# Performance work log

Measured on AMD Instinct MI355X. Metric: run time of the kernel, lower is better.

## Reference

```python
import jax, jax.numpy as jnp
import numpy as np

N = 50000        # nodes
E = 800000       # edges
FEAT = 64        # cfg.feature_dim
HID = 128        # cfg.hidden_dim
G = 8            # num graphs
EPS = 1e-5       # LayerNorm eps
MIN_DEPTH, MAX_DEPTH = 0.1, 3.0


def _ln(x, g, b):
    m = jnp.mean(x, axis=-1, keepdims=True)
    v = jnp.mean((x - m) ** 2, axis=-1, keepdims=True)
    return (x - m) * jax.lax.rsqrt(v + EPS) * g + b


def setup_inputs() -> dict:
    key = jax.random.key(0)
    ks = jax.random.split(key, 32)
    f32 = jnp.float32
    inp = {}
    inp['x'] = jax.random.normal(ks[0], (N, FEAT), dtype=f32)
    inp['edge_index'] = jax.random.randint(ks[1], (2, E), 0, N)
    inp['batch'] = jnp.sort(jax.random.randint(ks[2], (N,), 0, G))
    # input_projection: Linear(FEAT,HID) + LayerNorm
    inp['in_w'] = jax.random.normal(ks[3], (FEAT, HID), dtype=f32) * (1.0 / np.sqrt(FEAT))
    inp['in_b'] = jnp.zeros((HID,), f32)
    inp['in_ln_g'] = jnp.ones((HID,), f32)
    inp['in_ln_b'] = jnp.zeros((HID,), f32)
    # epigenetics
    inp['methylation'] = jnp.zeros((HID,), f32)
    inp['histones'] = jnp.zeros((4,), f32)
    inp['log_depth'] = jnp.zeros((), f32)
    # NeuralODEFunc: 3 stacked GCNConv(HID,HID) + LayerNorms, gate MLP, residual scalar
    inp['gcn_w'] = jax.random.normal(ks[4], (3, HID, HID), dtype=f32) * (1.0 / np.sqrt(HID))
    inp['gcn_b'] = jnp.zeros((3, HID), f32)
    inp['ln_g'] = jnp.ones((3, HID), f32)
    inp['ln_b'] = jnp.zeros((3, HID), f32)
    inp['gate_w'] = jax.random.normal(ks[5], (2 * HID, HID), dtype=f32) * (1.0 / np.sqrt(2 * HID))
    inp['gate_b'] = jnp.zeros((HID,), f32)
    inp['residual_weight'] = jnp.asarray(0.1, f32)
    # output_projection: Linear(HID,HID) + LayerNorm
    inp['out_w'] = jax.random.normal(ks[6], (HID, HID), dtype=f32) * (1.0 / np.sqrt(HID))
    inp['out_b'] = jnp.zeros((HID,), f32)
    inp['out_ln_g'] = jnp.ones((HID,), f32)
    inp['out_ln_b'] = jnp.zeros((HID,), f32)
    return inp


def reference(x, edge_index, batch, in_w, in_b, in_ln_g, in_ln_b, methylation,
              histones, log_depth, gcn_w, gcn_b, ln_g, ln_b, gate_w, gate_b,
              residual_weight, out_w, out_b, out_ln_g, out_ln_b):
    n = x.shape[0]
    src, dst = edge_index[0], edge_index[1]

    # input_projection (Dropout is identity in eval)
    h = jax.nn.relu(_ln(x @ in_w + in_b, in_ln_g, in_ln_b))

    # epigenetic regulation (chromatin_accessibility goes through .item() -> constant)
    meth_sil = jnp.mean(jax.nn.sigmoid(methylation))
    hm = jax.nn.sigmoid(histones)
    act = (hm[0] + hm[2]) * 0.5
    rep = (hm[1] + hm[3]) * 0.5
    chrom = jax.lax.stop_gradient(jnp.clip(act - rep + 0.5, 0.0, 1.0))
    h = h * (chrom * (1.0 - meth_sil))

    # symmetric GCN normalization, no self loops (computed once, no grad path)
    deg = jax.ops.segment_sum(jnp.ones((E,), h.dtype), dst, num_segments=n)
    dinv = jnp.where(deg > 0, jax.lax.rsqrt(jnp.maximum(deg, 1.0)), 0.0)
    enorm = (dinv[src] * dinv[dst])[:, None]  # [E,1]

    def gcn(hh, i):
        xw = hh @ gcn_w[i]                                   # [N,H]
        agg = jax.ops.segment_sum(xw[src] * enorm, dst, num_segments=n)
        return agg + gcn_b[i]

    def ode_f(hh):
        h_orig = hh
        cur = hh
        for i in range(3):  # fixed layer count
            h_new = _ln(gcn(cur, i), ln_g[i], ln_b[i])
            if i > 0:
                gate = jax.nn.sigmoid(
                    jnp.concatenate([cur, h_new], axis=-1) @ gate_w + gate_b)
                cur = gate * h_new + (1.0 - gate) * cur
            else:
                cur = h_new
        cur = jnp.tanh(cur)
        return cur + residual_weight * h_orig

    # depth via .item() in torch -> non-differentiable constant
    depth = jax.lax.stop_gradient(
        jnp.clip(jnp.exp(log_depth), MIN_DEPTH, MAX_DEPTH))
    # single fixed RK4 step over t = linspace(0, depth, 2)
    dt = depth
    k1 = ode_f(h)
    k2 = ode_f(h + 0.5 * dt * k1)
    k3 = ode_f(h + 0.5 * dt * k2)
    k4 = ode_f(h + dt * k3)
    h_final = h + (dt / 6.0) * (k1 + 2.0 * k2 + 2.0 * k3 + k4)

    # output_projection + global_mean_pool over batch
    h_out = _ln(h_final @ out_w + out_b, out_ln_g, out_ln_b)
    cnt = jax.ops.segment_sum(jnp.ones((n,), h.dtype), batch, num_segments=G)
    pooled = jax.ops.segment_sum(h_out, batch, num_segments=G)
    return pooled / jnp.maximum(cnt, 1.0)[:, None]
```

## Files before the change

kernel.cpp:

```cpp
#include <hip/hip_runtime.h>
#include <math.h>

#define NN 50000
#define EE 800000
#define HH 128
#define FF 64
#define GG 8
#define PB 500

using short8 = __attribute__((ext_vector_type(8))) short;
using f32x4  = __attribute__((ext_vector_type(4))) float;

__device__ __forceinline__ float sigm(float x){ return 1.0f/(1.0f+expf(-x)); }
__device__ __forceinline__ unsigned short f2bf(float f){
    union { float f; unsigned u; } v; v.f = f;
    unsigned r = v.u + 0x7fff + ((v.u >> 16) & 1);
    return (unsigned short)(r >> 16);
}
__device__ __forceinline__ float bf2f(unsigned short h){
    union { unsigned u; float f; } v; v.u = ((unsigned)h) << 16;
    return v.f;
}

__global__ void k_setup(const float* __restrict__ meth,
                        const float* __restrict__ histones,
                        const float* __restrict__ logd,
                        float* __restrict__ scal)
{
    int l = threadIdx.x;
    float s = sigm(meth[l]) + sigm(meth[l + 64]);
#pragma unroll
    for (int o = 32; o >= 1; o >>= 1) s += __shfl_xor(s, o, 64);
    if (l == 0) {
        float msil = s * (1.0f / 128.0f);
        float h0 = sigm(histones[0]), h1 = sigm(histones[1]);
        float h2 = sigm(histones[2]), h3 = sigm(histones[3]);
        float act = (h0 + h2) * 0.5f, rep = (h1 + h3) * 0.5f;
        float chrom = fminf(fmaxf(act - rep + 0.5f, 0.0f), 1.0f);
        scal[0] = chrom * (1.0f - msil);
        float d = expf(logd[0]);
        scal[1] = fminf(fmaxf(d, 0.1f), 3.0f);
    }
}

__global__ void k_pack(const float* __restrict__ W, unsigned short* __restrict__ out, int K)
{
    int i = blockIdx.x * 256 + threadIdx.x;
    if (i >= K * 128) return;
    int k = i >> 7, n = i & 127;
    int c = k >> 5, kl = k & 31, q = kl >> 3, j = kl & 7;
    int b = n >> 4, ln = n & 15;
    int lane = q * 16 + ln;
    out[((c * 8 + b) * 64 + lane) * 8 + j] = f2bf(W[i]);
}

__global__ void k_cvtx(const float* __restrict__ x, unsigned short* __restrict__ xb)
{
    size_t i = (size_t)blockIdx.x * 256 + threadIdx.x;
    if (i >= (size_t)NN * 16) return;
    float4 v = ((const float4*)x)[i];
    ushort4 o;
    o.x = f2bf(v.x); o.y = f2bf(v.y); o.z = f2bf(v.z); o.w = f2bf(v.w);
    ((ushort4*)xb)[i] = o;
}

__global__ void k_hist(const int* __restrict__ ei, int* __restrict__ hist)
{
    int e = blockIdx.x * 256 + threadIdx.x;
    if (e < EE) atomicAdd(&hist[ei[EE + e]], 1);
}

__global__ void k_dinv(const int* __restrict__ hist, float* __restrict__ dinv)
{
    int n = blockIdx.x * 256 + threadIdx.x;
    if (n < NN) {
        int d = hist[n];
        dinv[n] = d > 0 ? rsqrtf((float)d) : 0.0f;
    }
}

__global__ void k_scan_a(const int* __restrict__ hist, int* __restrict__ aux)
{
    __shared__ int sh[256];
    int b = blockIdx.x, t = threadIdx.x;
    int base = b * 1024 + t * 4;
    int s = 0;
#pragma unroll
    for (int j = 0; j < 4; ++j) { int i = base + j; if (i < NN) s += hist[i]; }
    sh[t] = s; __syncthreads();
    for (int o = 128; o >= 1; o >>= 1) { if (t < o) sh[t] += sh[t + o]; __syncthreads(); }
    if (t == 0) aux[b] = sh[0];
}

__global__ void k_scan_b(int* __restrict__ aux, int nb)
{
    if (blockIdx.x == 0 && threadIdx.x == 0) {
        int run = 0;
        for (int i = 0; i < nb; ++i) { int v = aux[i]; aux[i] = run; run += v; }
    }
}

__global__ void k_scan_c(const int* __restrict__ hist, const int* __restrict__ aux,
                         int* __restrict__ row_ptr)
{
    __shared__ int sh[256];
    int b = blockIdx.x, t = threadIdx.x;
    int base = b * 1024 + t * 4;
    int v[4]; int s = 0;
#pragma unroll
    for (int j = 0; j < 4; ++j) { int i = base + j; v[j] = (i < NN) ? hist[i] : 0; s += v[j]; }
    sh[t] = s; __syncthreads();
    for (int o = 1; o < 256; o <<= 1) {
        int x = 0; if (t >= o) x = sh[t - o];
        __syncthreads(); sh[t] += x; __syncthreads();
    }
    int run = aux[b] + sh[t] - s;
#pragma unroll
    for (int j = 0; j < 4; ++j) { int i = base + j; if (i < NN) row_ptr[i] = run; run += v[j]; }
    if (b == 0 && t == 0) row_ptr[NN] = EE;
}

__global__ void k_scatter(const int* __restrict__ ei, const float* __restrict__ dinv,
                          int* __restrict__ cursor, int2* __restrict__ ew)
{
    int e = blockIdx.x * 256 + threadIdx.x;
    if (e >= EE) return;
    int s = ei[e], d = ei[EE + e];
    int p = atomicAdd(&cursor[d], 1);
    ew[p] = make_int2(s, __float_as_int(dinv[s] * dinv[d]));
}

__global__ void k_bounds(const int* __restrict__ batch, int* __restrict__ st)
{
    int g = threadIdx.x;
    if (g > GG) return;
    int lo = 0, hi = NN;
    while (lo < hi) { int mid = (lo + hi) >> 1; if (batch[mid] < g) lo = mid + 1; else hi = mid; }
    st[g] = lo;
}

template<int KC, int MODE>
__global__ __launch_bounds__(256) void k_dense_mfma(
    const unsigned short* __restrict__ A, const unsigned short* __restrict__ Wp,
    const float* __restrict__ bias, const float* __restrict__ lng,
    const float* __restrict__ lnb, const float* __restrict__ scal,
    unsigned short* __restrict__ out)
{
    __shared__ unsigned short Ws[KC * 4096];
    const int t = threadIdx.x;
    {
        const float4* src = (const float4*)Wp;
        float4* dst = (float4*)Ws;
#pragma unroll
        for (int i = 0; i < KC * 2; ++i) dst[t + i * 256] = src[t + i * 256];
    }
    __syncthreads();
    const int wave = t >> 6, lane = t & 63;
    const int quad = lane >> 4, ln = lane & 15;
    const int r0 = blockIdx.x * 64 + wave * 16;
    const int K = KC * 32;
    const int arow = r0 + ln;
    const bool av = arow < NN;

    f32x4 acc[8] = {};
#pragma unroll
    for (int c = 0; c < KC; ++c) {
        short8 a = {};
        if (av) a = *(const short8*)(A + (size_t)arow * K + c * 32 + quad * 8);
#pragma unroll
        for (int b = 0; b < 8; ++b) {
            short8 bb = *(const short8*)&Ws[((c * 8 + b) * 64 + lane) * 8];
            acc[b] = __builtin_amdgcn_mfma_f32_16x16x32_bf16(a, bb, acc[b], 0, 0, 0);
        }
    }

    float b_s[8], g_s[8], e_s[8];
#pragma unroll
    for (int b = 0; b < 8; ++b) {
        int col = b * 16 + ln;
        b_s[b] = bias[col]; g_s[b] = lng[col]; e_s[b] = lnb[col];
    }
    float sc = (MODE == 1) ? scal[0] : 0.0f;
#pragma unroll
    for (int i = 0; i < 4; ++i) {
        int row = r0 + quad * 4 + i;
        float v[8]; float s = 0.f, q = 0.f;
#pragma unroll
        for (int b = 0; b < 8; ++b) { float x = acc[b][i] + b_s[b]; v[b] = x; s += x; q += x * x; }
#pragma unroll
        for (int o = 1; o < 16; o <<= 1) { s += __shfl_xor(s, o, 64); q += __shfl_xor(q, o, 64); }
        float m  = s * (1.0f / 128.0f);
        float vr = q * (1.0f / 128.0f) - m * m;
        float rs = rsqrtf(vr + 1e-5f);
        if (row < NN) {
#pragma unroll
            for (int b = 0; b < 8; ++b) {
                float o2 = (v[b] - m) * rs * g_s[b] + e_s[b];
                if (MODE == 1) o2 = fmaxf(o2, 0.f) * sc;
                out[(size_t)row * 128 + b * 16 + ln] = f2bf(o2);
            }
        }
    }
}

__global__ __launch_bounds__(256) void k_gate_mfma(
    unsigned short* __restrict__ cur, const unsigned short* __restrict__ hnew,
    const unsigned short* __restrict__ Wp, const float* __restrict__ gb)
{
    __shared__ unsigned short Ws[16384];
    const int t = threadIdx.x;
    const int wave = t >> 6, lane = t & 63;
    const int quad = lane >> 4, ln = lane & 15;
    const int r0 = blockIdx.x * 64 + wave * 16;
    const int arow = r0 + ln;
    const bool av = arow < NN;

    f32x4 acc[8] = {};
#pragma unroll
    for (int s = 0; s < 2; ++s) {
        __syncthreads();
        {
            const float4* src = (const float4*)(Wp + (size_t)s * 16384);
            float4* dst = (float4*)Ws;
#pragma unroll
            for (int i = 0; i < 8; ++i) dst[t + i * 256] = src[t + i * 256];
        }
        __syncthreads();
        const unsigned short* A = s ? hnew : cur;
#pragma unroll
        for (int c = 0; c < 4; ++c) {
            short8 a = {};
            if (av) a = *(const short8*)(A + (size_t)arow * 128 + c * 32 + quad * 8);
#pragma unroll
            for (int b = 0; b < 8; ++b) {
                short8 bb = *(const short8*)&Ws[((c * 8 + b) * 64 + lane) * 8];
                acc[b] = __builtin_amdgcn_mfma_f32_16x16x32_bf16(a, bb, acc[b], 0, 0, 0);
            }
        }
    }

    float gb_s[8];
#pragma unroll
    for (int b = 0; b < 8; ++b) gb_s[b] = gb[b * 16 + ln];
#pragma unroll
    for (int i = 0; i < 4; ++i) {
        int row = r0 + quad * 4 + i;
        if (row < NN) {
#pragma unroll
            for (int b = 0; b < 8; ++b) {
                size_t idx = (size_t)row * 128 + b * 16 + ln;
                float g  = sigm(acc[b][i] + gb_s[b]);
                float cu = bf2f(cur[idx]);
                float hn = bf2f(hnew[idx]);
                cur[idx] = f2bf(g * hn + (1.f - g) * cu);
            }
        }
    }
}

__global__ __launch_bounds__(256) void k_spmm(
    const int* __restrict__ rp, const int2* __restrict__ ew,
    const unsigned short* __restrict__ X, unsigned short* __restrict__ out)
{
    const int wave = threadIdx.x >> 6, lane = threadIdx.x & 63;
    const int node = blockIdx.x * 4 + wave;
    const int beg = rp[node], end = rp[node + 1];
    float2 acc = make_float2(0.f, 0.f);
    const unsigned short* Xl = X + lane * 2;

    for (int base = beg; base < end; base += 64) {
        const int cnt = min(64, end - base);
        int2 my = make_int2(0, 0);
        if (lane < cnt) my = ew[base + lane];
        const int cq = (cnt + 7) & ~7;
        for (int j = 0; j < cq; j += 8) {
            float2 v[8]; float wv[8];
#pragma unroll
            for (int u = 0; u < 8; ++u) {
                int s  = __shfl(my.x, j + u, 64);
                wv[u]  = __int_as_float(__shfl(my.y, j + u, 64));
                ushort2 r = *(const ushort2*)(Xl + (size_t)s * 128);
                v[u] = make_float2(bf2f(r.x), bf2f(r.y));
            }
#pragma unroll
            for (int u = 0; u < 8; ++u) {
                acc.x = fmaf(wv[u], v[u].x, acc.x);
                acc.y = fmaf(wv[u], v[u].y, acc.y);
            }
        }
    }
    ushort2 o; o.x = f2bf(acc.x); o.y = f2bf(acc.y);
    *(ushort2*)(out + (size_t)node * 128 + lane * 2) = o;
}

template<int S>
__global__ __launch_bounds__(256) void k_stage(
    const unsigned short* __restrict__ cur, const unsigned short* __restrict__ fin,
    const unsigned short* __restrict__ h0, float* __restrict__ acc,
    unsigned short* __restrict__ ybuf, const float* __restrict__ scal,
    const float* __restrict__ rwp)
{
    size_t i = (size_t)blockIdx.x * 256 + threadIdx.x;
    if (i >= (size_t)NN * 32) return;
    float dt = scal[1], rw = rwp[0];
    float wk = (S == 1 || S == 4) ? dt * (1.f / 6.f) : dt * (1.f / 3.f);
    ushort4 c4 = ((const ushort4*)cur)[i];
    ushort4 f4 = ((const ushort4*)fin)[i];
    ushort4 h4 = ((const ushort4*)h0)[i];
    float tv[4];
    tv[0] = tanhf(bf2f(c4.x)) + rw * bf2f(f4.x);
    tv[1] = tanhf(bf2f(c4.y)) + rw * bf2f(f4.y);
    tv[2] = tanhf(bf2f(c4.z)) + rw * bf2f(f4.z);
    tv[3] = tanhf(bf2f(c4.w)) + rw * bf2f(f4.w);
    float4 a;
    if (S == 1) { a.x = wk*tv[0]; a.y = wk*tv[1]; a.z = wk*tv[2]; a.w = wk*tv[3]; }
    else {
        a = ((const float4*)acc)[i];
        a.x += wk*tv[0]; a.y += wk*tv[1]; a.z += wk*tv[2]; a.w += wk*tv[3];
    }
    ((float4*)acc)[i] = a;
    float h[4] = { bf2f(h4.x), bf2f(h4.y), bf2f(h4.z), bf2f(h4.w) };
    ushort4 y;
    if (S == 4) {
        y.x = f2bf(h[0] + a.x); y.y = f2bf(h[1] + a.y);
        y.z = f2bf(h[2] + a.z); y.w = f2bf(h[3] + a.w);
    } else {
        float cn = (S == 3) ? dt : 0.5f * dt;
        y.x = f2bf(h[0] + cn*tv[0]); y.y = f2bf(h[1] + cn*tv[1]);
        y.z = f2bf(h[2] + cn*tv[2]); y.w = f2bf(h[3] + cn*tv[3]);
    }
    ((ushort4*)ybuf)[i] = y;
}

__global__ __launch_bounds__(128) void k_pool1(
    const unsigned short* __restrict__ h, const int* __restrict__ batch,
    float* __restrict__ partial)
{
    int c = threadIdx.x, b = blockIdx.x;
    int r0 = b * (NN / PB), r1 = r0 + (NN / PB);
    float acc = 0.f; int g = batch[r0];
#pragma unroll 4
    for (int r = r0; r < r1; ++r) {
        int gg = batch[r];
        if (gg != g) { partial[(size_t)b * 1024 + g * 128 + c] = acc; acc = 0.f; g = gg; }
        acc += bf2f(h[(size_t)r * 128 + c]);
    }
    partial[(size_t)b * 1024 + g * 128 + c] = acc;
}

__global__ __launch_bounds__(128) void k_pool2(
    const float* __restrict__ partial, const int* __restrict__ st,
    float* __restrict__ out)
{
    int g = blockIdx.x, c = threadIdx.x;
    float s = 0.f;
#pragma unroll 8
    for (int b = 0; b < PB; ++b) s += partial[(size_t)b * 1024 + g * 128 + c];
    int cnt = st[g + 1] - st[g];
    out[g * 128 + c] = s / (float)(cnt > 0 ? cnt : 1);
}

static inline size_t al(size_t x) { return (x + 255) & ~(size_t)255; }

extern "C" void kernel_launch(void* const* d_in, const int* in_sizes, int n_in,
                              void* d_out, int out_size, void* d_ws, size_t ws_size,
                              hipStream_t stream)
{
    const float* x       = (const float*)d_in[0];
    const int*   ei      = (const int*)d_in[1];
    const int*   batch   = (const int*)d_in[2];
    const float* in_w    = (const float*)d_in[3];
    const float* in_b    = (const float*)d_in[4];
    const float* in_lng  = (const float*)d_in[5];
    const float* in_lnb  = (const float*)d_in[6];
    const float* meth    = (const float*)d_in[7];
    const float* histn   = (const float*)d_in[8];
    const float* logd    = (const float*)d_in[9];
    const float* gcn_w   = (const float*)d_in[10];
    const float* gcn_b   = (const float*)d_in[11];
    const float* ln_g    = (const float*)d_in[12];
    const float* ln_b    = (const float*)d_in[13];
    const float* gate_w  = (const float*)d_in[14];
    const float* gate_b  = (const float*)d_in[15];
    const float* rw      = (const float*)d_in[16];
    const float* out_w   = (const float*)d_in[17];
    const float* out_b   = (const float*)d_in[18];
    const float* out_lng = (const float*)d_in[19];
    const float* out_lnb = (const float*)d_in[20];
    float* out = (float*)d_out;

    char* w = (char*)d_ws;
    size_t off = 0;
    float* scal   = (float*)(w + off); off += al(16 * 4);
    int*   hist   = (int*)(w + off);   off += al((size_t)NN * 4);
    int*   rp     = (int*)(w + off);   off += al((size_t)(NN + 1) * 4);
    int*   cursor = (int*)(w + off);   off += al((size_t)(NN + 1) * 4);
    int*   aux    = (int*)(w + off);   off += al(64 * 4);
    int*   st     = (int*)(w + off);   off += al(16 * 4);
    float* dinv   = (float*)(w + off); off += al((size_t)NN * 4);
    int2*  ew     = (int2*)(w + off);  off += al((size_t)EE * 8);
    float* partial= (float*)(w + off); off += al((size_t)PB * 1024 * 4);
    unsigned short* inwp  = (unsigned short*)(w + off); off += al(64 * 128 * 2);
    unsigned short* gcnwp = (unsigned short*)(w + off); off += al((size_t)3 * 128 * 128 * 2);
    unsigned short* gwp   = (unsigned short*)(w + off); off += al((size_t)2 * 128 * 128 * 2);
    unsigned short* owp   = (unsigned short*)(w + off); off += al(128 * 128 * 2);
    size_t B16 = al((size_t)NN * 128 * 2);
    unsigned short* xb  = (unsigned short*)(w + off); off += al((size_t)NN * 64 * 2);
    unsigned short* h0  = (unsigned short*)(w + off); off += B16;
    unsigned short* y   = (unsigned short*)(w + off); off += B16;
    unsigned short* cur = (unsigned short*)(w + off); off += B16;
    unsigned short* t1  = (unsigned short*)(w + off); off += B16;
    unsigned short* t2  = (unsigned short*)(w + off); off += B16;
    float* acc = (float*)(w + off); off += al((size_t)NN * 128 * 4);
    if (off > ws_size) return;

    hipMemsetAsync(hist, 0, (size_t)NN * 4, stream);
    hipMemsetAsync(partial, 0, (size_t)PB * 1024 * 4, stream);

    k_setup<<<1, 64, 0, stream>>>(meth, histn, logd, scal);
    k_pack<<<32, 256, 0, stream>>>(in_w, inwp, 64);
    for (int i = 0; i < 3; ++i)
        k_pack<<<64, 256, 0, stream>>>(gcn_w + (size_t)i * 128 * 128,
                                       gcnwp + (size_t)i * 128 * 128, 128);
    k_pack<<<64, 256, 0, stream>>>(gate_w, gwp, 128);
    k_pack<<<64, 256, 0, stream>>>(gate_w + 128 * 128, gwp + 128 * 128, 128);
    k_pack<<<64, 256, 0, stream>>>(out_w, owp, 128);
    k_cvtx<<<3125, 256, 0, stream>>>(x, xb);

    k_hist<<<(EE + 255) / 256, 256, 0, stream>>>(ei, hist);
    k_dinv<<<(NN + 255) / 256, 256, 0, stream>>>(hist, dinv);
    k_scan_a<<<49, 256, 0, stream>>>(hist, aux);
    k_scan_b<<<1, 1, 0, stream>>>(aux, 49);
    k_scan_c<<<49, 256, 0, stream>>>(hist, aux, rp);
    hipMemcpyAsync(cursor, rp, (size_t)(NN + 1) * 4, hipMemcpyDeviceToDevice, stream);
    k_scatter<<<(EE + 255) / 256, 256, 0, stream>>>(ei, dinv, cursor, ew);
    k_bounds<<<1, 16, 0, stream>>>(batch, st);

    const int DG = (NN + 63) / 64;
    k_dense_mfma<2, 1><<<DG, 256, 0, stream>>>(xb, inwp, in_b, in_lng, in_lnb, scal, h0);

    for (int s = 1; s <= 4; ++s) {
        const unsigned short* fin = (s == 1) ? h0 : y;
        k_spmm<<<12500, 256, 0, stream>>>(rp, ew, fin, t1);
        k_dense_mfma<4, 0><<<DG, 256, 0, stream>>>(t1, gcnwp, gcn_b, ln_g, ln_b, scal, cur);
        for (int i = 1; i <= 2; ++i) {
            k_spmm<<<12500, 256, 0, stream>>>(rp, ew, cur, t1);
            k_dense_mfma<4, 0><<<DG, 256, 0, stream>>>(
                t1, gcnwp + (size_t)i * 128 * 128, gcn_b + i * 128,
                ln_g + i * 128, ln_b + i * 128, scal, t2);
            k_gate_mfma<<<DG, 256, 0, stream>>>(cur, t2, gwp, gate_b);
        }
        if (s == 1)      k_stage<1><<<6250, 256, 0, stream>>>(cur, fin, h0, acc, y, scal, rw);
        else if (s == 2) k_stage<2><<<6250, 256, 0, stream>>>(cur, fin, h0, acc, y, scal, rw);
        else if (s == 3) k_stage<3><<<6250, 256, 0, stream>>>(cur, fin, h0, acc, y, scal, rw);
        else             k_stage<4><<<6250, 256, 0, stream>>>(cur, fin, h0, acc, y, scal, rw);
    }

    k_dense_mfma<4, 0><<<DG, 256, 0, stream>>>(y, owp, out_b, out_lng, out_lnb, scal, t2);
    k_pool1<<<PB, 128, 0, stream>>>(t2, batch, partial);
    k_pool2<<<GG, 128, 0, stream>>>(partial, st, out);
}
```

Measured before the change: 934.8 us.

## Fuse sparse aggregation with GCN dense MFMA and LayerNorm into one kernel

Replaces the separate SpMM kernel and dense MFMA kernel with a single k_spgemm. Each block aggregates neighbor features for 64 destination nodes into an LDS fp32 tile using a packed edge format (16-bit src plus local dst index), then runs the MFMA matmul and LayerNorm directly on that tile. This removes the bf16 t1 intermediate round trip and a kernel launch per layer. It also drops the LDS weight staging in the dense and gate kernels in favour of direct global reads, and splits pool2 across more blocks. The 16-bit src packing only holds because N is 50000, and each wave now walks its 16 nodes' edges serially, which lowers gather parallelism compared with one wave per node.

```diff
diff --git a/kernel.cpp b/kernel.cpp
--- a/kernel.cpp
+++ b/kernel.cpp
@@ -121,13 +121,14 @@
 }
 
 __global__ void k_scatter(const int* __restrict__ ei, const float* __restrict__ dinv,
-                          int* __restrict__ cursor, int2* __restrict__ ew)
+                          int* __restrict__ cursor, uint2* __restrict__ ew)
 {
     int e = blockIdx.x * 256 + threadIdx.x;
     if (e >= EE) return;
     int s = ei[e], d = ei[EE + e];
     int p = atomicAdd(&cursor[d], 1);
-    ew[p] = make_int2(s, __float_as_int(dinv[s] * dinv[d]));
+    ew[p] = make_uint2((unsigned)(s & 0xFFFF) | ((unsigned)(d & 63) << 16),
+                       __float_as_uint(dinv[s] * dinv[d]));
 }
 
 __global__ void k_bounds(const int* __restrict__ batch, int* __restrict__ st)
@@ -146,16 +147,7 @@
     const float* __restrict__ lnb, const float* __restrict__ scal,
     unsigned short* __restrict__ out)
 {
-    __shared__ unsigned short Ws[KC * 4096];
-    const int t = threadIdx.x;
-    {
-        const float4* src = (const float4*)Wp;
-        float4* dst = (float4*)Ws;
-#pragma unroll
-        for (int i = 0; i < KC * 2; ++i) dst[t + i * 256] = src[t + i * 256];
-    }
-    __syncthreads();
-    const int wave = t >> 6, lane = t & 63;
+    const int t = threadIdx.x, wave = t >> 6, lane = t & 63;
     const int quad = lane >> 4, ln = lane & 15;
     const int r0 = blockIdx.x * 64 + wave * 16;
     const int K = KC * 32;
@@ -169,7 +161,7 @@
         if (av) a = *(const short8*)(A + (size_t)arow * K + c * 32 + quad * 8);
 #pragma unroll
         for (int b = 0; b < 8; ++b) {
-            short8 bb = *(const short8*)&Ws[((c * 8 + b) * 64 + lane) * 8];
+            short8 bb = *(const short8*)(Wp + ((size_t)(c * 8 + b) * 64 + lane) * 8);
             acc[b] = __builtin_amdgcn_mfma_f32_16x16x32_bf16(a, bb, acc[b], 0, 0, 0);
         }
     }
@@ -203,11 +195,109 @@
     }
 }
 
+__global__ __launch_bounds__(256) void k_spgemm(
+    const int* __restrict__ rp, const uint2* __restrict__ ew,
+    const unsigned short* __restrict__ X, const unsigned short* __restrict__ Wp,
+    const float* __restrict__ bias, const float* __restrict__ lng,
+    const float* __restrict__ lnb, unsigned short* __restrict__ out)
+{
+    __shared__ float accf[64 * 132];
+    const int t = threadIdx.x, wave = t >> 6, lane = t & 63;
+    const int quad = lane >> 4, ln = lane & 15;
+    const int n0 = blockIdx.x * 64;
+    const int nf = n0 + wave * 16;
+
+    {
+        float* z = accf + wave * 16 * 132;
+        for (int i = lane; i < 16 * 132; i += 64) z[i] = 0.f;
+    }
+
+    if (nf < NN) {
+        const int nl = min(nf + 16, NN);
+        const int ebeg = __builtin_amdgcn_readfirstlane(rp[nf]);
+        const int eend = __builtin_amdgcn_readfirstlane(rp[nl]);
+        if (ebeg < eend) {
+            float2 racc = make_float2(0.f, 0.f);
+            int curd = (int)((ew[ebeg].x >> 16) & 63u);
+            const unsigned short* Xl = X + lane * 2;
+            for (int e = ebeg; e < eend; e += 8) {
+                const int m = min(8, eend - e);
+                uint2 r[8]; float2 g[8];
+#pragma unroll
+                for (int u = 0; u < 8; ++u) r[u] = ew[e + u];
+#pragma unroll
+                for (int u = 0; u < 8; ++u) {
+                    int src = (int)(r[u].x & 0xFFFFu);
+                    ushort2 v = *(const ushort2*)(Xl + (size_t)src * 128);
+                    g[u] = make_float2(bf2f(v.x), bf2f(v.y));
+                }
+#pragma unroll
+                for (int u = 0; u < 8; ++u) {
+                    if (u >= m) break;
+                    int dl = (int)((r[u].x >> 16) & 63u);
+                    float wt = __uint_as_float(r[u].y);
+                    if (dl != curd) {
+                        *(float2*)&accf[curd * 132 + lane * 2] = racc;
+                        racc = make_float2(0.f, 0.f);
+                        curd = dl;
+                    }
+                    racc.x = fmaf(wt, g[u].x, racc.x);
+                    racc.y = fmaf(wt, g[u].y, racc.y);
+                }
+            }
+            *(float2*)&accf[curd * 132 + lane * 2] = racc;
+        }
+    }
+
+    f32x4 acc[8] = {};
+    const float* ar = accf + ((size_t)(wave * 16 + ln)) * 132;
+#pragma unroll
+    for (int c = 0; c < 4; ++c) {
+        float4 a0 = *(const float4*)(ar + c * 32 + quad * 8);
+        float4 a1 = *(const float4*)(ar + c * 32 + quad * 8 + 4);
+        short8 af;
+        af[0] = (short)f2bf(a0.x); af[1] = (short)f2bf(a0.y);
+        af[2] = (short)f2bf(a0.z); af[3] = (short)f2bf(a0.w);
+        af[4] = (short)f2bf(a1.x); af[5] = (short)f2bf(a1.y);
+        af[6] = (short)f2bf(a1.z); af[7] = (short)f2bf(a1.w);
+#pragma unroll
+        for (int b = 0; b < 8; ++b) {
+            short8 bb = *(const short8*)(Wp + ((size_t)(c * 8 + b) * 64 + lane) * 8);
+            acc[b] = __builtin_amdgcn_mfma_f32_16x16x32_bf16(af, bb, acc[b], 0, 0, 0);
+        }
+    }
+
+    float b_s[8], g_s[8], e_s[8];
+#pragma unroll
+    for (int b = 0; b < 8; ++b) {
+        int col = b * 16 + ln;
+        b_s[b] = bias[col]; g_s[b] = lng[col]; e_s[b] = lnb[col];
+    }
+#pragma unroll
+    for (int i = 0; i < 4; ++i) {
+        int row = n0 + wave * 16 + quad * 4 + i;
+        float v[8]; float s = 0.f, q = 0.f;
+#pragma unroll
+        for (int b = 0; b < 8; ++b) { float x = acc[b][i] + b_s[b]; v[b] = x; s += x; q += x * x; }
+#pragma unroll
+        for (int o = 1; o < 16; o <<= 1) { s += __shfl_xor(s, o, 64); q += __shfl_xor(q, o, 64); }
+        float m  = s * (1.0f / 128.0f);
+        float vr = q * (1.0f / 128.0f) - m * m;
+        float rs = rsqrtf(vr + 1e-5f);
+        if (row < NN) {
+#pragma unroll
+            for (int b = 0; b < 8; ++b) {
+                float o2 = (v[b] - m) * rs * g_s[b] + e_s[b];
+                out[(size_t)row * 128 + b * 16 + ln] = f2bf(o2);
+            }
+        }
+    }
+}
+
 __global__ __launch_bounds__(256) void k_gate_mfma(
     unsigned short* __restrict__ cur, const unsigned short* __restrict__ hnew,
     const unsigned short* __restrict__ Wp, const float* __restrict__ gb)
 {
-    __shared__ unsigned short Ws[16384];
     const int t = threadIdx.x;
     const int wave = t >> 6, lane = t & 63;
     const int quad = lane >> 4, ln = lane & 15;
@@ -218,22 +308,15 @@
     f32x4 acc[8] = {};
 #pragma unroll
     for (int s = 0; s < 2; ++s) {
-        __syncthreads();
-        {
-            const float4* src = (const float4*)(Wp + (size_t)s * 16384);
-            float4* dst = (float4*)Ws;
-#pragma unroll
-            for (int i = 0; i < 8; ++i) dst[t + i * 256] = src[t + i * 256];
-        }
-        __syncthreads();
         const unsigned short* A = s ? hnew : cur;
+        const unsigned short* Wh = Wp + (size_t)s * 16384;
 #pragma unroll
         for (int c = 0; c < 4; ++c) {
             short8 a = {};
             if (av) a = *(const short8*)(A + (size_t)arow * 128 + c * 32 + quad * 8);
 #pragma unroll
             for (int b = 0; b < 8; ++b) {
-                short8 bb = *(const short8*)&Ws[((c * 8 + b) * 64 + lane) * 8];
+                short8 bb = *(const short8*)(Wh + ((size_t)(c * 8 + b) * 64 + lane) * 8);
                 acc[b] = __builtin_amdgcn_mfma_f32_16x16x32_bf16(a, bb, acc[b], 0, 0, 0);
             }
         }
@@ -256,41 +339,6 @@
             }
         }
     }
-}
-
-__global__ __launch_bounds__(256) void k_spmm(
-    const int* __restrict__ rp, const int2* __restrict__ ew,
-    const unsigned short* __restrict__ X, unsigned short* __restrict__ out)
-{
-    const int wave = threadIdx.x >> 6, lane = threadIdx.x & 63;
-    const int node = blockIdx.x * 4 + wave;
-    const int beg = rp[node], end = rp[node + 1];
-    float2 acc = make_float2(0.f, 0.f);
-    const unsigned short* Xl = X + lane * 2;
-
-    for (int base = beg; base < end; base += 64) {
-        const int cnt = min(64, end - base);
-        int2 my = make_int2(0, 0);
-        if (lane < cnt) my = ew[base + lane];
-        const int cq = (cnt + 7) & ~7;
-        for (int j = 0; j < cq; j += 8) {
-            float2 v[8]; float wv[8];
-#pragma unroll
-            for (int u = 0; u < 8; ++u) {
-                int s  = __shfl(my.x, j + u, 64);
-                wv[u]  = __int_as_float(__shfl(my.y, j + u, 64));
-                ushort2 r = *(const ushort2*)(Xl + (size_t)s * 128);
-                v[u] = make_float2(bf2f(r.x), bf2f(r.y));
-            }
-#pragma unroll
-            for (int u = 0; u < 8; ++u) {
-                acc.x = fmaf(wv[u], v[u].x, acc.x);
-                acc.y = fmaf(wv[u], v[u].y, acc.y);
-            }
-        }
-    }
-    ushort2 o; o.x = f2bf(acc.x); o.y = f2bf(acc.y);
-    *(ushort2*)(out + (size_t)node * 128 + lane * 2) = o;
 }
 
 template<int S>
@@ -348,16 +396,24 @@
     partial[(size_t)b * 1024 + g * 128 + c] = acc;
 }
 
-__global__ __launch_bounds__(128) void k_pool2(
+__global__ __launch_bounds__(256) void k_pool2(
     const float* __restrict__ partial, const int* __restrict__ st,
     float* __restrict__ out)
 {
-    int g = blockIdx.x, c = threadIdx.x;
+    __shared__ float sh[8][32];
+    int cb = blockIdx.x & 3, g = blockIdx.x >> 2;
+    int cl = threadIdx.x & 31, sl = threadIdx.x >> 5;
+    int c = cb * 32 + cl;
     float s = 0.f;
-#pragma unroll 8
-    for (int b = 0; b < PB; ++b) s += partial[(size_t)b * 1024 + g * 128 + c];
-    int cnt = st[g + 1] - st[g];
-    out[g * 128 + c] = s / (float)(cnt > 0 ? cnt : 1);
+    for (int b = sl; b < PB; b += 8) s += partial[(size_t)b * 1024 + g * 128 + c];
+    sh[sl][cl] = s; __syncthreads();
+    if (sl == 0) {
+        float tt = 0.f;
+#pragma unroll
+        for (int i = 0; i < 8; ++i) tt += sh[i][cl];
+        int cnt = st[g + 1] - st[g];
+        out[g * 128 + c] = tt / (float)(cnt > 0 ? cnt : 1);
+    }
 }
 
 static inline size_t al(size_t x) { return (x + 255) & ~(size_t)255; }
@@ -398,7 +454,7 @@
     int*   aux    = (int*)(w + off);   off += al(64 * 4);
     int*   st     = (int*)(w + off);   off += al(16 * 4);
     float* dinv   = (float*)(w + off); off += al((size_t)NN * 4);
-    int2*  ew     = (int2*)(w + off);  off += al((size_t)EE * 8);
+    uint2* ew     = (uint2*)(w + off); off += al((size_t)(EE + 8) * 8);
     float* partial= (float*)(w + off); off += al((size_t)PB * 1024 * 4);
     unsigned short* inwp  = (unsigned short*)(w + off); off += al(64 * 128 * 2);
     unsigned short* gcnwp = (unsigned short*)(w + off); off += al((size_t)3 * 128 * 128 * 2);
@@ -409,13 +465,13 @@
     unsigned short* h0  = (unsigned short*)(w + off); off += B16;
     unsigned short* y   = (unsigned short*)(w + off); off += B16;
     unsigned short* cur = (unsigned short*)(w + off); off += B16;
-    unsigned short* t1  = (unsigned short*)(w + off); off += B16;
     unsigned short* t2  = (unsigned short*)(w + off); off += B16;
     float* acc = (float*)(w + off); off += al((size_t)NN * 128 * 4);
     if (off > ws_size) return;
 
     hipMemsetAsync(hist, 0, (size_t)NN * 4, stream);
     hipMemsetAsync(partial, 0, (size_t)PB * 1024 * 4, stream);
+    hipMemsetAsync(ew + EE, 0, 8 * sizeof(uint2), stream);
 
     k_setup<<<1, 64, 0, stream>>>(meth, histn, logd, scal);
     k_pack<<<32, 256, 0, stream>>>(in_w, inwp, 64);
@@ -441,13 +497,11 @@
 
     for (int s = 1; s <= 4; ++s) {
         const unsigned short* fin = (s == 1) ? h0 : y;
-        k_spmm<<<12500, 256, 0, stream>>>(rp, ew, fin, t1);
-        k_dense_mfma<4, 0><<<DG, 256, 0, stream>>>(t1, gcnwp, gcn_b, ln_g, ln_b, scal, cur);
+        k_spgemm<<<DG, 256, 0, stream>>>(rp, ew, fin, gcnwp, gcn_b, ln_g, ln_b, cur);
         for (int i = 1; i <= 2; ++i) {
-            k_spmm<<<12500, 256, 0, stream>>>(rp, ew, cur, t1);
-            k_dense_mfma<4, 0><<<DG, 256, 0, stream>>>(
-                t1, gcnwp + (size_t)i * 128 * 128, gcn_b + i * 128,
-                ln_g + i * 128, ln_b + i * 128, scal, t2);
+            k_spgemm<<<DG, 256, 0, stream>>>(rp, ew, cur,
+                                             gcnwp + (size_t)i * 128 * 128, gcn_b + i * 128,
+                                             ln_g + i * 128, ln_b + i * 128, t2);
             k_gate_mfma<<<DG, 256, 0, stream>>>(cur, t2, gwp, gate_b);
         }
         if (s == 1)      k_stage<1><<<6250, 256, 0, stream>>>(cur, fin, h0, acc, y, scal, rw);
@@ -458,5 +512,5 @@
 
     k_dense_mfma<4, 0><<<DG, 256, 0, stream>>>(y, owp, out_b, out_lng, out_lnb, scal, t2);
     k_pool1<<<PB, 128, 0, stream>>>(t2, batch, partial);
-    k_pool2<<<GG, 128, 0, stream>>>(partial, st, out);
-}
+    k_pool2<<<GG * 4, 256, 0, stream>>>(partial, st, out);
+}
```

Result: slower. 1.032 ms (+10.4%).
